# Kernel tuning notes

Measured on AMD Instinct MI355X. Metric: run time of the kernel, lower is better.

The kernel has to match this reference:

```python
import jax, jax.numpy as jnp
import numpy as np

N_NODES = 100000
N_EDGES = 1600000
D = 64  # latent = hidden = output = 64


def gcn_conv(x, W, b, src, dst, n):
    # PyG GCNConv: out = D^{-1/2} (A + I) D^{-1/2} (x W) + b, self-loops added.
    h = x @ W  # [N, d_out]
    ones = jnp.ones(src.shape[0], dtype=h.dtype)
    deg = jax.ops.segment_sum(ones, dst, num_segments=n) + 1.0  # +1 for self-loop
    dinv = jax.lax.rsqrt(deg)  # [N]
    norm = dinv[src] * dinv[dst]  # [E]
    msgs = h[src] * norm[:, None]  # gather + scale, [E, d_out]
    agg = jax.ops.segment_sum(msgs, dst, num_segments=n)  # scatter-add
    # self-loop contribution: dinv[i]^2 * h[i]
    agg = agg + h * (dinv * dinv)[:, None]
    return agg + b


def setup_inputs() -> dict:
    key = jax.random.key(0)
    ks = jax.random.split(key, 9)
    s = 1.0 / np.sqrt(D)
    return {
        "z": jax.random.normal(ks[0], (N_NODES, D), dtype=jnp.float32),
        "src": jax.random.randint(ks[1], (N_EDGES,), 0, N_NODES, dtype=jnp.int32),
        "dst": jax.random.randint(ks[2], (N_EDGES,), 0, N_NODES, dtype=jnp.int32),
        "W1": jax.random.uniform(ks[3], (D, D), jnp.float32, -s, s),
        "b1": jnp.zeros((D,), jnp.float32),
        "W2": jax.random.uniform(ks[4], (D, D), jnp.float32, -s, s),
        "b2": jnp.zeros((D,), jnp.float32),
        "W3": jax.random.uniform(ks[5], (D, D), jnp.float32, -s, s),
        "b3": jnp.zeros((D,), jnp.float32),
    }


def reference(z, src, dst, W1, b1, W2, b2, W3, b3):
    n = z.shape[0]
    x = jax.nn.relu(gcn_conv(z, W1, b1, src, dst, n))
    x = jax.nn.relu(gcn_conv(x, W2, b2, src, dst, n))
    x = gcn_conv(x, W3, b3, src, dst, n)
    return x
```

## Files before the change

### kernel.cpp

```cpp
#include <hip/hip_runtime.h>
#include <hip/hip_fp16.h>

#define N_NODES 100000
#define N_EDGES 1600000
#define N_BUCKETS 256
#define BUCKET_NODES 391
#define BKT_BLOCKS 512
#define CAP_E 8192
#define CAP_C 12288
#define DUMMY N_NODES

typedef unsigned short u16;
typedef _Float16 f16x8 __attribute__((ext_vector_type(8)));
typedef float f32x4 __attribute__((ext_vector_type(4)));

__device__ __forceinline__ u16 f2h(float f) {
    return __half_as_ushort(__float2half_rn(f));
}

__device__ __forceinline__ void acc8(float* acc, uint4 q) {
    unsigned v[4] = {q.x, q.y, q.z, q.w};
#pragma unroll
    for (int i = 0; i < 4; ++i) {
        __half2 h = *reinterpret_cast<__half2*>(&v[i]);
        float2 f = __half22float2(h);
        acc[2 * i] += f.x;
        acc[2 * i + 1] += f.y;
    }
}

__global__ __launch_bounds__(256) void k_bucket(const int* __restrict__ src,
                                                const int* __restrict__ dst,
                                                int* __restrict__ btot,
                                                int* __restrict__ ebuf) {
    __shared__ int cnt[N_BUCKETS], base_s[N_BUCKETS];
    const int CS = N_EDGES / BKT_BLOCKS;
    int t = threadIdx.x;
    int beg = blockIdx.x * CS, end = beg + CS;
    for (int i = t; i < N_BUCKETS; i += 256) cnt[i] = 0;
    __syncthreads();
    for (int e = beg + t; e < end; e += 256)
        atomicAdd(&cnt[(unsigned)dst[e] / BUCKET_NODES], 1);
    __syncthreads();
    for (int i = t; i < N_BUCKETS; i += 256) {
        base_s[i] = atomicAdd(&btot[i], cnt[i]);
        cnt[i] = 0;
    }
    __syncthreads();
    for (int e = beg + t; e < end; e += 256) {
        int d = dst[e], s = src[e];
        int b = (unsigned)d / BUCKET_NODES;
        int l = atomicAdd(&cnt[b], 1);
        ebuf[b * CAP_E + base_s[b] + l] = s | ((d - b * BUCKET_NODES) << 17);
    }
}

__global__ __launch_bounds__(1024) void k_build(const int* __restrict__ btot,
                                                const int* __restrict__ ebuf,
                                                int* __restrict__ col,
                                                int2* __restrict__ rowinfo,
                                                float* __restrict__ dinv,
                                                const float* __restrict__ z,
                                                u16* __restrict__ xs,
                                                u16* __restrict__ xs_other) {
    __shared__ int deg[BUCKET_NODES];
    __shared__ int cur[BUCKET_NODES];
    __shared__ int sm[512];
    __shared__ int cls[CAP_C];
    int b = blockIdx.x, t = threadIdx.x;
    int nb = b * BUCKET_NODES;
    int nn = N_NODES - nb < BUCKET_NODES ? N_NODES - nb : BUCKET_NODES;
    int ne = btot[b];
    const int* eb = ebuf + b * CAP_E;

    for (int i = t; i < BUCKET_NODES; i += 1024) deg[i] = 0;
    __syncthreads();
    for (int e = t; e < ne; e += 1024) atomicAdd(&deg[eb[e] >> 17], 1);
    __syncthreads();

    int v = (t < nn) ? ((deg[t] + 7) & ~7) : 0;
    if (t < 512) sm[t] = v;
    __syncthreads();
    for (int off = 1; off < 512; off <<= 1) {
        int u = (t >= off && t < 512) ? sm[t - off] : 0;
        __syncthreads();
        if (t < 512) sm[t] += u;
        __syncthreads();
    }
    int total = sm[511];
    int colbase = b * CAP_C;
    if (t < nn) {
        int off0 = sm[t] - v;
        cur[t] = off0;
        rowinfo[nb + t] = make_int2(colbase + off0, v);
        dinv[nb + t] = rsqrtf((float)deg[t] + 1.0f);
    }
    __syncthreads();
    for (int i = t; i < total; i += 1024) cls[i] = DUMMY << 7;
    __syncthreads();
    for (int e = t; e < ne; e += 1024) {
        int pe = eb[e];
        int l = atomicAdd(&cur[pe >> 17], 1);
        cls[l] = (pe & 0x1FFFF) << 7;
    }
    __syncthreads();
    for (int i = t; i < total; i += 1024) col[colbase + i] = cls[i];
    if (t < 16) col[colbase + total + t] = DUMMY << 7;

    const float4* zz = (const float4*)(z + (size_t)nb * 64);
    uint2* xx = (uint2*)(xs + (size_t)nb * 64);
    for (int i = t; i < nn * 16; i += 1024) {
        float4 vv = zz[i];
        float dd = rsqrtf((float)deg[i >> 4] + 1.0f);
        unsigned p0 = (unsigned)f2h(vv.x * dd) | ((unsigned)f2h(vv.y * dd) << 16);
        unsigned p1 = (unsigned)f2h(vv.z * dd) | ((unsigned)f2h(vv.w * dd) << 16);
        xx[i] = make_uint2(p0, p1);
    }
    if (b == 0 && t < 8) {
        ((uint4*)(xs + (size_t)N_NODES * 64))[t] = make_uint4(0, 0, 0, 0);
        ((uint4*)(xs_other + (size_t)N_NODES * 64))[t] = make_uint4(0, 0, 0, 0);
    }
}

__global__ __launch_bounds__(256) void k_agg(const int2* __restrict__ rowinfo,
                                             const int* __restrict__ col,
                                             const float* __restrict__ dinv,
                                             const u16* __restrict__ xs,
                                             u16* __restrict__ h) {
    const int lane = threadIdx.x & 63;
    const int eighth = lane >> 3;
    const int fh = lane & 7;
    const char* xb = (const char*)xs;
    int wave = (blockIdx.x * blockDim.x + threadIdx.x) >> 6;
    int nwaves = (gridDim.x * blockDim.x) >> 6;

    for (int n0 = wave * 2; n0 < N_NODES; n0 += nwaves * 2) {
        int u0 = __builtin_amdgcn_readfirstlane(n0);
        int u1 = u0 + 1;
        bool has1 = (u1 < N_NODES);
        int2 r0 = rowinfo[u0];
        int2 r1 = has1 ? rowinfo[u1] : r0;
        int it0 = r0.y >> 4, it1 = r1.y >> 4;
        int itm = it0 > it1 ? it0 : it1;

        float a0[8] = {0.f, 0.f, 0.f, 0.f, 0.f, 0.f, 0.f, 0.f};
        float a1[8] = {0.f, 0.f, 0.f, 0.f, 0.f, 0.f, 0.f, 0.f};
        for (int r = 0; r < itm; ++r) {
            int oo0 = (r < it0) ? (r << 4) : 0;
            int oo1 = (r < it1) ? (r << 4) : 0;
            int2 c0 = *(const int2*)(col + r0.x + oo0 + 2 * eighth);
            int2 c1 = *(const int2*)(col + r1.x + oo1 + 2 * eighth);
            uint4 qa = *(const uint4*)(xb + (unsigned)c0.x + fh * 16);
            uint4 qb = *(const uint4*)(xb + (unsigned)c0.y + fh * 16);
            uint4 qc = *(const uint4*)(xb + (unsigned)c1.x + fh * 16);
            uint4 qd = *(const uint4*)(xb + (unsigned)c1.y + fh * 16);
            if (r < it0) { acc8(a0, qa); acc8(a0, qb); }
            if (r < it1) { acc8(a1, qc); acc8(a1, qd); }
        }
        int t0 = (r0.y >> 3) & 1, t1 = (r1.y >> 3) & 1;
        if (t0 | t1) {
            int s0 = col[r0.x + (it0 << 4) + eighth];
            int s1 = col[r1.x + (it1 << 4) + eighth];
            uint4 q0 = *(const uint4*)(xb + (unsigned)s0 + fh * 16);
            uint4 q1 = *(const uint4*)(xb + (unsigned)s1 + fh * 16);
            if (t0) acc8(a0, q0);
            if (t1) acc8(a1, q1);
        }

        uint4 qs0 = *(const uint4*)(xb + (size_t)u0 * 128 + fh * 16);
        uint4 qs1 = *(const uint4*)(xb + (size_t)u1 * 128 + fh * 16);
        float d0 = dinv[u0];
        float d1 = has1 ? dinv[u1] : 0.f;

#pragma unroll
        for (int m = 8; m <= 32; m <<= 1) {
#pragma unroll
            for (int j = 0; j < 8; ++j) {
                a0[j] += __shfl_xor(a0[j], m, 64);
                a1[j] += __shfl_xor(a1[j], m, 64);
            }
        }
        float s0[8] = {0.f, 0.f, 0.f, 0.f, 0.f, 0.f, 0.f, 0.f};
        float s1[8] = {0.f, 0.f, 0.f, 0.f, 0.f, 0.f, 0.f, 0.f};
        acc8(s0, qs0); acc8(s1, qs1);
        uint4 p0, p1;
        u16* pp0 = (u16*)&p0;
        u16* pp1 = (u16*)&p1;
#pragma unroll
        for (int j = 0; j < 8; ++j) {
            pp0[j] = f2h((a0[j] + s0[j]) * d0);
            pp1[j] = f2h((a1[j] + s1[j]) * d1);
        }
        if (eighth == 0) ((uint4*)(h + (size_t)u0 * 64))[fh] = p0;
        if (has1 && eighth == 1) ((uint4*)(h + (size_t)u1 * 64))[fh] = p1;
    }
}

__global__ __launch_bounds__(256) void k_mv(const u16* __restrict__ h,
                                            const float* __restrict__ W,
                                            const float* __restrict__ bias,
                                            const float* __restrict__ dinv,
                                            u16* __restrict__ outh,
                                            float* __restrict__ outf, int hidden) {
    const int lane = threadIdx.x & 63;
    const int quad = lane >> 4;
    const int l16 = lane & 15;

    f16x8 bfr[4][2];
#pragma unroll
    for (int t = 0; t < 4; ++t)
#pragma unroll
        for (int c = 0; c < 2; ++c)
#pragma unroll
            for (int j = 0; j < 8; ++j)
                bfr[t][c][j] = (_Float16)W[(quad * 8 + 32 * c + j) * 64 + l16 + 16 * t];
    float bv[4];
#pragma unroll
    for (int t = 0; t < 4; ++t) bv[t] = bias[l16 + 16 * t];

    int wave = (blockIdx.x * blockDim.x + threadIdx.x) >> 6;
    int nwaves = (gridDim.x * blockDim.x) >> 6;
    for (int chunk = wave; chunk < N_NODES / 16; chunk += nwaves) {
        int row0 = chunk * 16;
        const u16* hb = h + (size_t)row0 * 64;
        union { uint4 u; f16x8 f; } a0, a1;
        a0.u = *(const uint4*)(hb + l16 * 64 + quad * 8);
        a1.u = *(const uint4*)(hb + l16 * 64 + quad * 8 + 32);

        f32x4 acc[4] = {{0.f, 0.f, 0.f, 0.f}, {0.f, 0.f, 0.f, 0.f},
                        {0.f, 0.f, 0.f, 0.f}, {0.f, 0.f, 0.f, 0.f}};
#pragma unroll
        for (int t = 0; t < 4; ++t) {
            acc[t] = __builtin_amdgcn_mfma_f32_16x16x32_f16(a0.f, bfr[t][0], acc[t], 0, 0, 0);
            acc[t] = __builtin_amdgcn_mfma_f32_16x16x32_f16(a1.f, bfr[t][1], acc[t], 0, 0, 0);
        }
        float dv[4];
#pragma unroll
        for (int r = 0; r < 4; ++r) dv[r] = dinv[row0 + quad * 4 + r];
#pragma unroll
        for (int r = 0; r < 4; ++r) {
            int row = row0 + quad * 4 + r;
#pragma unroll
            for (int t = 0; t < 4; ++t) {
                float o = acc[t][r] + bv[t];
                if (hidden) {
                    o = fmaxf(o, 0.f) * dv[r];
                    outh[(size_t)row * 64 + l16 + 16 * t] = f2h(o);
                } else {
                    outf[(size_t)row * 64 + l16 + 16 * t] = o;
                }
            }
        }
    }
}

extern "C" void kernel_launch(void* const* d_in, const int* in_sizes, int n_in,
                              void* d_out, int out_size, void* d_ws, size_t ws_size,
                              hipStream_t stream) {
    const float* z  = (const float*)d_in[0];
    const int* src  = (const int*)d_in[1];
    const int* dst  = (const int*)d_in[2];
    const float* W1 = (const float*)d_in[3];
    const float* b1 = (const float*)d_in[4];
    const float* W2 = (const float*)d_in[5];
    const float* b2 = (const float*)d_in[6];
    const float* W3 = (const float*)d_in[7];
    const float* b3 = (const float*)d_in[8];
    float* out = (float*)d_out;

    char* p = (char*)d_ws;
    float* dinv    = (float*)p;  p += (size_t)512 << 10;
    int2*  rowinfo = (int2*)p;   p += (size_t)1 << 20;
    int*   btot    = (int*)p;    p += (size_t)4 << 10;
    int*   ebuf    = (int*)p;    p += (size_t)N_BUCKETS * CAP_E * 4;
    int*   col     = (int*)p;    p += (size_t)N_BUCKETS * CAP_C * 4;
    u16*   hbuf    = (u16*)p;    p += (size_t)13 << 20;
    u16*   buf0    = (u16*)p;    p += (size_t)13 << 20;
    u16*   buf1    = (u16*)p;

    const int gA = 2048;
    const int gM = 512;

    hipMemsetAsync(btot, 0, N_BUCKETS * sizeof(int), stream);
    k_bucket<<<BKT_BLOCKS, 256, 0, stream>>>(src, dst, btot, ebuf);
    k_build<<<N_BUCKETS, 1024, 0, stream>>>(btot, ebuf, col, rowinfo, dinv, z, buf0, buf1);

    k_agg<<<gA, 256, 0, stream>>>(rowinfo, col, dinv, buf0, hbuf);
    k_mv <<<gM, 256, 0, stream>>>(hbuf, W1, b1, dinv, buf1, nullptr, 1);
    k_agg<<<gA, 256, 0, stream>>>(rowinfo, col, dinv, buf1, hbuf);
    k_mv <<<gM, 256, 0, stream>>>(hbuf, W2, b2, dinv, buf0, nullptr, 1);
    k_agg<<<gA, 256, 0, stream>>>(rowinfo, col, dinv, buf0, hbuf);
    k_mv <<<gM, 256, 0, stream>>>(hbuf, W3, b3, dinv, nullptr, out, 0);
}
```

Measured before the change: 266.6 us.

## Split node features into four 16-channel planes for cache-friendly gather

```diff
diff --git a/kernel.cpp b/kernel.cpp
--- a/kernel.cpp
+++ b/kernel.cpp
@@ -9,6 +9,7 @@
 #define CAP_E 8192
 #define CAP_C 12288
 #define DUMMY N_NODES
+#define CH_ELE ((size_t)(N_NODES + 8) * 16)
 
 typedef unsigned short u16;
 typedef _Float16 f16x8 __attribute__((ext_vector_type(8)));
@@ -96,29 +97,32 @@
         dinv[nb + t] = rsqrtf((float)deg[t] + 1.0f);
     }
     __syncthreads();
-    for (int i = t; i < total; i += 1024) cls[i] = DUMMY << 7;
+    for (int i = t; i < total; i += 1024) cls[i] = DUMMY << 5;
     __syncthreads();
     for (int e = t; e < ne; e += 1024) {
         int pe = eb[e];
         int l = atomicAdd(&cur[pe >> 17], 1);
-        cls[l] = (pe & 0x1FFFF) << 7;
+        cls[l] = (pe & 0x1FFFF) << 5;
     }
     __syncthreads();
     for (int i = t; i < total; i += 1024) col[colbase + i] = cls[i];
-    if (t < 16) col[colbase + total + t] = DUMMY << 7;
+    if (t < 16) col[colbase + total + t] = DUMMY << 5;
 
     const float4* zz = (const float4*)(z + (size_t)nb * 64);
-    uint2* xx = (uint2*)(xs + (size_t)nb * 64);
     for (int i = t; i < nn * 16; i += 1024) {
         float4 vv = zz[i];
+        int node = nb + (i >> 4);
+        int c = (i & 15) >> 2;
+        int q = i & 3;
         float dd = rsqrtf((float)deg[i >> 4] + 1.0f);
         unsigned p0 = (unsigned)f2h(vv.x * dd) | ((unsigned)f2h(vv.y * dd) << 16);
         unsigned p1 = (unsigned)f2h(vv.z * dd) | ((unsigned)f2h(vv.w * dd) << 16);
-        xx[i] = make_uint2(p0, p1);
-    }
-    if (b == 0 && t < 8) {
-        ((uint4*)(xs + (size_t)N_NODES * 64))[t] = make_uint4(0, 0, 0, 0);
-        ((uint4*)(xs_other + (size_t)N_NODES * 64))[t] = make_uint4(0, 0, 0, 0);
+        *(uint2*)(xs + (size_t)c * CH_ELE + (size_t)node * 16 + q * 4) = make_uint2(p0, p1);
+    }
+    if (b == 0 && t < 16) {
+        int c = t >> 2, q = t & 3;
+        *(uint2*)(xs + (size_t)c * CH_ELE + (size_t)DUMMY * 16 + q * 4) = make_uint2(0, 0);
+        *(uint2*)(xs_other + (size_t)c * CH_ELE + (size_t)DUMMY * 16 + q * 4) = make_uint2(0, 0);
     }
 }
 
@@ -128,71 +132,57 @@
                                              const u16* __restrict__ xs,
                                              u16* __restrict__ h) {
     const int lane = threadIdx.x & 63;
-    const int eighth = lane >> 3;
-    const int fh = lane & 7;
-    const char* xb = (const char*)xs;
+    const int g = lane >> 5;
+    const int slot = (lane & 31) >> 1;
+    const int hh = lane & 1;
     int wave = (blockIdx.x * blockDim.x + threadIdx.x) >> 6;
     int nwaves = (gridDim.x * blockDim.x) >> 6;
 
-    for (int n0 = wave * 2; n0 < N_NODES; n0 += nwaves * 2) {
-        int u0 = __builtin_amdgcn_readfirstlane(n0);
-        int u1 = u0 + 1;
-        bool has1 = (u1 < N_NODES);
-        int2 r0 = rowinfo[u0];
-        int2 r1 = has1 ? rowinfo[u1] : r0;
-        int it0 = r0.y >> 4, it1 = r1.y >> 4;
-        int itm = it0 > it1 ? it0 : it1;
-
-        float a0[8] = {0.f, 0.f, 0.f, 0.f, 0.f, 0.f, 0.f, 0.f};
-        float a1[8] = {0.f, 0.f, 0.f, 0.f, 0.f, 0.f, 0.f, 0.f};
-        for (int r = 0; r < itm; ++r) {
-            int oo0 = (r < it0) ? (r << 4) : 0;
-            int oo1 = (r < it1) ? (r << 4) : 0;
-            int2 c0 = *(const int2*)(col + r0.x + oo0 + 2 * eighth);
-            int2 c1 = *(const int2*)(col + r1.x + oo1 + 2 * eighth);
-            uint4 qa = *(const uint4*)(xb + (unsigned)c0.x + fh * 16);
-            uint4 qb = *(const uint4*)(xb + (unsigned)c0.y + fh * 16);
-            uint4 qc = *(const uint4*)(xb + (unsigned)c1.x + fh * 16);
-            uint4 qd = *(const uint4*)(xb + (unsigned)c1.y + fh * 16);
-            if (r < it0) { acc8(a0, qa); acc8(a0, qb); }
-            if (r < it1) { acc8(a1, qc); acc8(a1, qd); }
+    for (int c = 0; c < 4; ++c) {
+        const char* xc = (const char*)(xs + (size_t)c * CH_ELE);
+        for (int n0 = wave * 2; n0 < N_NODES; n0 += nwaves * 2) {
+            int u0 = __builtin_amdgcn_readfirstlane(n0);
+            int u1 = u0 + 1;
+            int2 r0 = rowinfo[u0];
+            int2 r1 = rowinfo[u1];
+            int rbase = g ? r1.x : r0.x;
+            int y = g ? r1.y : r0.y;
+            int it = y >> 4;
+            int it0 = r0.y >> 4, it1 = r1.y >> 4;
+            int itm = it0 > it1 ? it0 : it1;
+
+            float acc[8] = {0.f, 0.f, 0.f, 0.f, 0.f, 0.f, 0.f, 0.f};
+            for (int r = 0; r < itm; ++r) {
+                int oo = (r < it) ? (r << 4) : 0;
+                int coff = col[rbase + oo + slot];
+                uint4 q = *(const uint4*)(xc + (unsigned)coff + hh * 16);
+                if (r < it) acc8(acc, q);
+            }
+            int tl = (y >> 3) & 1;
+            if (((r0.y | r1.y) >> 3) & 1) {
+                int coff = col[rbase + (it << 4) + (slot & 7)];
+                uint4 q = *(const uint4*)(xc + (unsigned)coff + hh * 16);
+                if (tl && slot < 8) acc8(acc, q);
+            }
+
+#pragma unroll
+            for (int m = 2; m <= 16; m <<= 1) {
+#pragma unroll
+                for (int j = 0; j < 8; ++j) acc[j] += __shfl_xor(acc[j], m, 64);
+            }
+
+            int un = g ? u1 : u0;
+            uint4 qs = *(const uint4*)(xc + (size_t)un * 32 + hh * 16);
+            float s[8] = {0.f, 0.f, 0.f, 0.f, 0.f, 0.f, 0.f, 0.f};
+            acc8(s, qs);
+            float dv = dinv[un];
+            uint4 p;
+            u16* pp = (u16*)&p;
+#pragma unroll
+            for (int j = 0; j < 8; ++j) pp[j] = f2h((acc[j] + s[j]) * dv);
+            if ((lane & 31) < 2)
+                *(uint4*)(h + (size_t)un * 64 + c * 16 + hh * 8) = p;
         }
-        int t0 = (r0.y >> 3) & 1, t1 = (r1.y >> 3) & 1;
-        if (t0 | t1) {
-            int s0 = col[r0.x + (it0 << 4) + eighth];
-            int s1 = col[r1.x + (it1 << 4) + eighth];
-            uint4 q0 = *(const uint4*)(xb + (unsigned)s0 + fh * 16);
-            uint4 q1 = *(const uint4*)(xb + (unsigned)s1 + fh * 16);
-            if (t0) acc8(a0, q0);
-            if (t1) acc8(a1, q1);
-        }
-
-        uint4 qs0 = *(const uint4*)(xb + (size_t)u0 * 128 + fh * 16);
-        uint4 qs1 = *(const uint4*)(xb + (size_t)u1 * 128 + fh * 16);
-        float d0 = dinv[u0];
-        float d1 = has1 ? dinv[u1] : 0.f;
-
-#pragma unroll
-        for (int m = 8; m <= 32; m <<= 1) {
-#pragma unroll
-            for (int j = 0; j < 8; ++j) {
-                a0[j] += __shfl_xor(a0[j], m, 64);
-                a1[j] += __shfl_xor(a1[j], m, 64);
-            }
-        }
-        float s0[8] = {0.f, 0.f, 0.f, 0.f, 0.f, 0.f, 0.f, 0.f};
-        float s1[8] = {0.f, 0.f, 0.f, 0.f, 0.f, 0.f, 0.f, 0.f};
-        acc8(s0, qs0); acc8(s1, qs1);
-        uint4 p0, p1;
-        u16* pp0 = (u16*)&p0;
-        u16* pp1 = (u16*)&p1;
-#pragma unroll
-        for (int j = 0; j < 8; ++j) {
-            pp0[j] = f2h((a0[j] + s0[j]) * d0);
-            pp1[j] = f2h((a1[j] + s1[j]) * d1);
-        }
-        if (eighth == 0) ((uint4*)(h + (size_t)u0 * 64))[fh] = p0;
-        if (has1 && eighth == 1) ((uint4*)(h + (size_t)u1 * 64))[fh] = p1;
     }
 }
 
@@ -245,7 +235,7 @@
                 float o = acc[t][r] + bv[t];
                 if (hidden) {
                     o = fmaxf(o, 0.f) * dv[r];
-                    outh[(size_t)row * 64 + l16 + 16 * t] = f2h(o);
+                    outh[(size_t)t * CH_ELE + (size_t)row * 16 + l16] = f2h(o);
                 } else {
                     outf[(size_t)row * 64 + l16 + 16 * t] = o;
                 }
```

Result: slower. 420.0 us (+57.5%).
